# Performance work log

Hardware: AMD Instinct MI355X
Metric: run time of the kernel (lower is better)

The kernel has to match this reference:

```python
import jax, jax.numpy as jnp
import numpy as np
import math

B, T, C, H = 4, 2048, 512, 8
HD = C // H


def make_alibias(block_size, ms):
    # ALiBi-style per-head bias: -m_h * |i - j|, shape [1, H, S, S]
    idx = jnp.arange(block_size)
    dist = jnp.abs(idx[:, None] - idx[None, :]).astype(jnp.float32)  # [S,S]
    return -ms[None, :, None, None] * dist[None, None, :, :]


def setup_inputs() -> dict:
    key = jax.random.key(0)
    k1, k2, k3, k4, k5 = jax.random.split(key, 5)
    x = jax.random.normal(k1, (B, T, C), dtype=jnp.float32)
    Wqkv = jax.random.normal(k2, (C, 3 * C), dtype=jnp.float32) * (1.0 / math.sqrt(C))
    bqkv = jax.random.normal(k3, (3 * C,), dtype=jnp.float32) * 0.02
    Wproj = jax.random.normal(k4, (C, C), dtype=jnp.float32) * (1.0 / math.sqrt(C))
    bproj = jax.random.normal(k5, (C,), dtype=jnp.float32) * 0.02
    ms = jnp.arange(1, H + 1, dtype=jnp.float32) * 0.05
    alibias = make_alibias(T, ms)  # [1,H,T,T]
    return {"x": x, "Wqkv": Wqkv, "bqkv": bqkv, "Wproj": Wproj, "bproj": bproj, "alibias": alibias}


def reference(x, Wqkv, bqkv, Wproj, bproj, alibias):
    Bv, Tv, Cv = x.shape
    qkv = x @ Wqkv + bqkv                      # [B,T,3C]
    q, k, v = jnp.split(qkv, 3, axis=-1)
    # [B,T,C] -> [B,H,T,hd]
    def heads(t):
        return t.reshape(Bv, Tv, H, HD).transpose(0, 2, 1, 3)
    q, k, v = heads(q), heads(k), heads(v)
    att = jnp.einsum('bhqd,bhkd->bhqk', q, k) * (1.0 / math.sqrt(HD))
    att = att + alibias[:, :, :Tv, :Tv]
    att = jax.nn.softmax(att, axis=-1)
    y = jnp.einsum('bhqk,bhkd->bhqd', att, v)  # [B,H,T,hd]
    y = y.transpose(0, 2, 1, 3).reshape(Bv, Tv, Cv)
    return y @ Wproj + bproj
```

## Files before the change

### kernel.cpp

```cpp
#include <hip/hip_runtime.h>
#include <hip/hip_bf16.h>

#define LOG2E 1.4426950408889634f

typedef __attribute__((ext_vector_type(8))) short short8;
typedef __attribute__((ext_vector_type(8))) __bf16 bf16x8;
typedef __attribute__((ext_vector_type(4))) float f32x4;

__device__ __forceinline__ unsigned short f2b(float f){
  unsigned int u = __builtin_bit_cast(unsigned int, f);
  u += 0x7fffu + ((u >> 16) & 1u);
  return (unsigned short)(u >> 16);
}

__device__ __forceinline__ unsigned int cvtpk(float lo, float hi){
  unsigned int r;
  asm("v_cvt_pk_bf16_f32 %0, %1, %2" : "=v"(r) : "v"(lo), "v"(hi));
  return r;
}

__device__ __forceinline__ void gload16(const void* g, void* l){
  __builtin_amdgcn_global_load_lds(
      (const __attribute__((address_space(1))) unsigned int*)g,
      (__attribute__((address_space(3))) unsigned int*)l, 16, 0, 0);
}

__global__ __launch_bounds__(256) void prep_kernel(
    const float* __restrict__ x, const float* __restrict__ Wqkv, const float* __restrict__ Wproj,
    unsigned short* __restrict__ xb, unsigned short* __restrict__ wqkvT, unsigned short* __restrict__ wprojT){
  __shared__ unsigned short T[64][72];
  const int bid = blockIdx.x, tid = threadIdx.x;
  if (bid < 2048){
    size_t i = ((size_t)bid * 256 + tid) * 8;
    float4 a = *(const float4*)(x + i);
    float4 b = *(const float4*)(x + i + 4);
    short8 s;
    s[0]=(short)f2b(a.x); s[1]=(short)f2b(a.y); s[2]=(short)f2b(a.z); s[3]=(short)f2b(a.w);
    s[4]=(short)f2b(b.x); s[5]=(short)f2b(b.y); s[6]=(short)f2b(b.z); s[7]=(short)f2b(b.w);
    *(short8*)(xb + i) = s;
    return;
  }
  const float* in; unsigned short* out; int R, C, bx, by;
  if (bid < 2240){ int t = bid - 2048; bx = t % 24; by = t / 24; in = Wqkv; out = wqkvT; R = 512; C = 1536; }
  else           { int t = bid - 2240; bx = t % 8;  by = t / 8;  in = Wproj; out = wprojT; R = 512; C = 512; }
  const int r0 = by * 64, c0 = bx * 64;
  {
    const int i = tid >> 2, jg = (tid & 3) * 16;
    const float* src = in + (size_t)(r0 + i) * C + c0 + jg;
    #pragma unroll
    for (int e = 0; e < 16; e += 4){
      float4 v = *(const float4*)(src + e);
      T[i][jg + e + 0] = f2b(v.x);
      T[i][jg + e + 1] = f2b(v.y);
      T[i][jg + e + 2] = f2b(v.z);
      T[i][jg + e + 3] = f2b(v.w);
    }
  }
  __syncthreads();
  {
    const int j = tid >> 2, ig = (tid & 3) * 16;
    short8 w0, w1;
    #pragma unroll
    for (int e = 0; e < 8; e++) w0[e] = (short)T[ig + e][j];
    #pragma unroll
    for (int e = 0; e < 8; e++) w1[e] = (short)T[ig + 8 + e][j];
    unsigned short* dst = out + (size_t)(c0 + j) * R + r0 + ig;
    *(short8*)dst = w0;
    *(short8*)(dst + 8) = w1;
  }
}

__global__ __launch_bounds__(256,3) void gemm_qkv_kernel(
    const unsigned short* __restrict__ A,
    const unsigned short* __restrict__ Bt,
    const float* __restrict__ bias,
    unsigned short* __restrict__ Qb,
    unsigned short* __restrict__ Kb,
    unsigned short* __restrict__ VTb,
    float* __restrict__ Mq, float* __restrict__ Mk){
  __shared__ unsigned short As[128*64];
  __shared__ unsigned short Bs[128*64];
  const int tid = threadIdx.x, wid = tid >> 6, lane = tid & 63;
  const int wr = wid >> 1, wc = wid & 1;
  const int fr = lane & 15, fq = lane >> 4;
  const int fr7 = fr & 7;
  const int orig = blockIdx.x;
  const int xcd = orig & 7, idx = orig >> 3;
  const int bm = (xcd + 8*(idx/12)) * 128;
  const int bn = (idx % 12) * 128;
  f32x4 acc[4][4];
  #pragma unroll
  for (int m=0;m<4;m++)
    #pragma unroll
    for (int n=0;n<4;n++) acc[m][n] = (f32x4){0.f,0.f,0.f,0.f};

  for (int k0 = 0; k0 < 512; k0 += 64){
    __syncthreads();
    #pragma unroll
    for (int it=0; it<4; it++){
      const int s = it*256 + tid;
      const int row = s >> 3, c = s & 7;
      const int sc = c ^ (row & 7);
      void* al = (void*)(As + (it*256 + wid*64)*8);
      void* bl = (void*)(Bs + (it*256 + wid*64)*8);
      gload16(A  + (size_t)(bm + row)*512 + k0 + sc*8, al);
      gload16(Bt + (size_t)(bn + row)*512 + k0 + sc*8, bl);
    }
    __syncthreads();
    bf16x8 af[4][2], bfv[4][2];
    #pragma unroll
    for (int m=0;m<4;m++)
      #pragma unroll
      for (int kk=0;kk<2;kk++)
        af[m][kk]  = *(const bf16x8*)&As[(wr*64 + m*16 + fr)*64 + (((kk*4+fq)^fr7)*8)];
    #pragma unroll
    for (int n=0;n<4;n++)
      #pragma unroll
      for (int kk=0;kk<2;kk++)
        bfv[n][kk] = *(const bf16x8*)&Bs[(wc*64 + n*16 + fr)*64 + (((kk*4+fq)^fr7)*8)];
    #pragma unroll
    for (int kk=0;kk<2;kk++)
      #pragma unroll
      for (int m=0;m<4;m++)
        #pragma unroll
        for (int n=0;n<4;n++)
          acc[m][n] = __builtin_amdgcn_mfma_f32_16x16x32_bf16(af[m][kk], bfv[n][kk], acc[m][n], 0,0,0);
  }

  const float SCQ = 0.125f * LOG2E;
  const int colbase = bn + wc*64;
  const int which = colbase >> 9;
  float ss[4][4];
  #pragma unroll
  for (int m=0;m<4;m++)
    #pragma unroll
    for (int g=0;g<4;g++) ss[m][g] = 0.f;

  #pragma unroll
  for (int m=0;m<4;m++){
    const int row0 = bm + wr*64 + m*16 + fq*4;
    const int b_ = row0 >> 11, t_ = row0 & 2047;
    #pragma unroll
    for (int n=0;n<4;n++){
      const int col = colbase + n*16 + fr;
      const int c = col & 511, hh = c >> 6, dd = c & 63;
      const float bv = bias[col];
      if (which == 0){
        #pragma unroll
        for (int g=0; g<4; g++){
          const float v = (acc[m][n][g] + bv) * SCQ;
          ss[m][g] = fmaf(v, v, ss[m][g]);
          Qb[((size_t)(b_*8 + hh)*2048 + t_ + g)*64 + dd] = f2b(v);
        }
      } else if (which == 1){
        #pragma unroll
        for (int g=0; g<4; g++){
          const float v = acc[m][n][g] + bv;
          ss[m][g] = fmaf(v, v, ss[m][g]);
          Kb[((size_t)(b_*8 + hh)*2048 + t_ + g)*64 + dd] = f2b(v);
        }
      } else {
        uint2 pk;
        pk.x = cvtpk(acc[m][n][0] + bv, acc[m][n][1] + bv);
        pk.y = cvtpk(acc[m][n][2] + bv, acc[m][n][3] + bv);
        *(uint2*)&VTb[((size_t)(b_*8 + hh)*64 + dd)*2048 + t_] = pk;
      }
    }
  }

  if (which <= 1){
    #pragma unroll
    for (int m=0;m<4;m++)
      #pragma unroll
      for (int g=0;g<4;g++){
        float s = ss[m][g];
        s += __shfl_xor(s, 1); s += __shfl_xor(s, 2);
        s += __shfl_xor(s, 4); s += __shfl_xor(s, 8);
        ss[m][g] = s;
      }
    float mx = 0.f;
    #pragma unroll
    for (int m=0;m<4;m++)
      #pragma unroll
      for (int g=0;g<4;g++) mx = fmaxf(mx, ss[m][g]);
    mx = fmaxf(mx, __shfl_xor(mx, 16));
    mx = fmaxf(mx, __shfl_xor(mx, 32));
    if (lane == 0){
      const int rowbase = bm + wr*64;
      const int b_ = rowbase >> 11, qc_ = (rowbase >> 6) & 31;
      const int h_ = (colbase >> 6) & 7;
      float* M = which ? Mk : Mq;
      M[(b_*8 + h_)*32 + qc_] = sqrtf(mx) * 1.01f;
    }
  }
}

__global__ __launch_bounds__(256,3) void attn_kernel(
    const unsigned short* __restrict__ Q,
    const unsigned short* __restrict__ K,
    const unsigned short* __restrict__ VT,
    const float* __restrict__ alib,
    const float* __restrict__ Mqa,
    const float* __restrict__ Mka,
    unsigned short* __restrict__ Y){
  __shared__ unsigned short Ks[2][64*64];
  __shared__ unsigned short Vs[2][64*64];
  __shared__ unsigned short Ps[4][16][72];
  __shared__ float MkS[32];
  __shared__ float wred[4];
  __shared__ int lst[32];
  __shared__ int nsh;
  const int tid = threadIdx.x, wid = tid >> 6, lane = tid & 63;
  const int fr = lane & 15, fq = lane >> 4;
  const int fr7 = fr & 7;
  const int id = blockIdx.x;
  const int h = id >> 7;
  const int low3 = id & 7, idx4 = (id & 127) >> 3;
  const int b = idx4 >> 2, off = idx4 & 3;
  const int quad = (low3 - b) & 7;
  const int qc = quad*4 + off;
  const int bh = b*8 + h;
  const int q0 = qc*64 + wid*16;
  const unsigned short* Qp = Q  + (size_t)bh * 131072;
  const unsigned short* Kp = K  + (size_t)bh * 131072;
  const unsigned short* Vp = VT + (size_t)bh * 131072;
  const float nmh2 = alib[(size_t)h * 4194304 + 1] * LOG2E;
  const float MqMk0 = Mqa[bh*32 + qc];
  if (tid < 32) MkS[tid] = Mka[bh*32 + tid];

  bf16x8 qf[2];
  #pragma unroll
  for (int kk=0;kk<2;kk++)
    qf[kk] = *(const bf16x8*)(Qp + (size_t)(q0 + fr)*64 + kk*32 + fq*8);

  bf16x8 ones;
  #pragma unroll
  for (int e=0;e<8;e++) ones[e] = __builtin_bit_cast(__bf16, (unsigned short)0x3F80);

  f32x4 o[4], osum;
  #pragma unroll
  for (int ni=0;ni<4;ni++) o[ni] = (f32x4){0.f,0.f,0.f,0.f};
  osum = (f32x4){0.f,0.f,0.f,0.f};
  float mr = -1e30f;
  const float qi = (float)(q0 + fr);
  const float qb = nmh2 * qi;
  f32x4 ka[4];
  #pragma unroll
  for (int ni=0;ni<4;ni++)
    #pragma unroll
    for (int g=0;g<4;g++) ka[ni][g] = nmh2 * (float)(ni*16 + fq*4 + g);

  auto stage = [&](int kt, int buf){
    const int kb = kt * 64;
    #pragma unroll
    for (int it=0; it<2; it++){
      const int s = it*256 + tid;
      const int row = s >> 3, c = s & 7;
      const int sc = c ^ (row & 7);
      gload16(Kp + (size_t)(kb + row)*64 + sc*8, (void*)(Ks[buf] + (it*256 + wid*64)*8));
      gload16(Vp + (size_t)row*2048 + kb + sc*8, (void*)(Vs[buf] + (it*256 + wid*64)*8));
    }
  };

  auto compute = [&](int kt, int buf, bool diag){
    const int kb = kt * 64;
    const unsigned short* KsB = Ks[buf];
    const unsigned short* VsB = Vs[buf];
    bf16x8 kf[4][2], vf[4][2];
    #pragma unroll
    for (int ni=0;ni<4;ni++)
      #pragma unroll
      for (int kk=0;kk<2;kk++){
        const int r = ni*16 + fr;
        const int sw = ((kk*4 + fq) ^ fr7) * 8;
        kf[ni][kk] = *(const bf16x8*)&KsB[r*64 + sw];
        vf[ni][kk] = *(const bf16x8*)&VsB[r*64 + sw];
      }

    f32x4 st[4];
    const f32x4 fz = {0.f,0.f,0.f,0.f};
    #pragma unroll
    for (int ni=0;ni<4;ni++){
      f32x4 t0 = __builtin_amdgcn_mfma_f32_16x16x32_bf16(kf[ni][0], qf[0], fz, 0,0,0);
      st[ni] = __builtin_amdgcn_mfma_f32_16x16x32_bf16(kf[ni][1], qf[1], t0, 0,0,0);
    }

    float cadd;
    if (diag){
      const float base = qi - (float)(kb + fq*4);
      #pragma unroll
      for (int ni=0;ni<4;ni++)
        #pragma unroll
        for (int g=0;g<4;g++){
          const float d = fabsf(base - (float)(ni*16 + g));
          st[ni][g] = fmaf(nmh2, d, st[ni][g]);
        }
      cadd = 0.f;
    } else {
      const float s1 = (kt > qc) ? 1.f : -1.f;
      #pragma unroll
      for (int ni=0;ni<4;ni++)
        #pragma unroll
        for (int g=0;g<4;g++)
          st[ni][g] = fmaf(s1, ka[ni][g], st[ni][g]);
      cadd = s1 * (nmh2 * (float)kb - qb);
    }

    float m0 = fmaxf(fmaxf(st[0][0], st[0][1]), fmaxf(st[0][2], st[0][3]));
    float m1 = fmaxf(fmaxf(st[1][0], st[1][1]), fmaxf(st[1][2], st[1][3]));
    float m2 = fmaxf(fmaxf(st[2][0], st[2][1]), fmaxf(st[2][2], st[2][3]));
    float m3 = fmaxf(fmaxf(st[3][0], st[3][1]), fmaxf(st[3][2], st[3][3]));
    float tm = fmaxf(fmaxf(m0, m1), fmaxf(m2, m3));
    tm = fmaxf(tm, __shfl_xor(tm, 16));
    tm = fmaxf(tm, __shfl_xor(tm, 32));
    const float tmt = tm + cadd;

    const bool nog = __all(tmt <= mr);
    float mn = mr, sc;
    if (!nog){
      mn = fmaxf(mr, tmt);
      sc = exp2f(mr - mn);
      mr = mn;
    }
    const float mexp = mn - cadd;
    #pragma unroll
    for (int ni=0;ni<4;ni++)
      #pragma unroll
      for (int g=0;g<4;g++)
        st[ni][g] = exp2f(st[ni][g] - mexp);

    if (!nog){
      #pragma unroll
      for (int g=0;g<4;g++){
        const float sv = __shfl(sc, fq*4 + g);
        #pragma unroll
        for (int ni=0;ni<4;ni++) o[ni][g] *= sv;
        osum[g] *= sv;
      }
    }
    #pragma unroll
    for (int ni=0;ni<4;ni++){
      uint2 pk;
      pk.x = cvtpk(st[ni][0], st[ni][1]);
      pk.y = cvtpk(st[ni][2], st[ni][3]);
      *(uint2*)&Ps[wid][fr][ni*16 + fq*4] = pk;
    }

    bf16x8 pf[2];
    #pragma unroll
    for (int kk=0;kk<2;kk++)
      pf[kk] = *(const bf16x8*)&Ps[wid][fr][kk*32 + fq*8];
    #pragma unroll
    for (int ni=0;ni<4;ni++){
      o[ni] = __builtin_amdgcn_mfma_f32_16x16x32_bf16(pf[0], vf[ni][0], o[ni], 0,0,0);
      o[ni] = __builtin_amdgcn_mfma_f32_16x16x32_bf16(pf[1], vf[ni][1], o[ni], 0,0,0);
    }
    osum = __builtin_amdgcn_mfma_f32_16x16x32_bf16(pf[0], ones, osum, 0,0,0);
    osum = __builtin_amdgcn_mfma_f32_16x16x32_bf16(pf[1], ones, osum, 0,0,0);
  };

  const int e0 = (qc + 1 < 32) ? qc + 1 : qc - 1;
  const int e1 = (qc + 1 < 32 && qc - 1 >= 0) ? qc - 1 : -1;
  stage(qc, 0);
  stage(e0, 1);
  asm volatile("s_waitcnt vmcnt(4)" ::: "memory");
  __builtin_amdgcn_sched_barrier(0);
  __builtin_amdgcn_s_barrier();
  compute(qc, 0, true);

  float wm = mr;
  #pragma unroll
  for (int d=1; d<16; d<<=1) wm = fminf(wm, __shfl_xor(wm, d));
  if (lane == 0) wred[wid] = wm;
  __syncthreads();
  const float thresh  = fminf(fminf(wred[0], wred[1]), fminf(wred[2], wred[3])) - 14.0f;
  const float threshW = wm - 14.0f;

  if (tid == 0){
    float maxMk = 0.f;
    #pragma unroll
    for (int t=0; t<32; t++) maxMk = fmaxf(maxMk, MkS[t]);
    int n = 0;
    if (e1 >= 0) lst[n++] = e1;
    for (int dt = 2; dt < 32; dt++){
      const float biasmax = nmh2 * (float)((dt - 1)*64 + 1);
      if (MqMk0 * maxMk + biasmax < thresh) break;
      int kt = qc + dt;
      if (kt < 32 && MqMk0 * MkS[kt] + biasmax >= thresh) lst[n++] = kt;
      kt = qc - dt;
      if (kt >= 0 && MqMk0 * MkS[kt] + biasmax >= thresh) lst[n++] = kt;
    }
    nsh = n;
  }
  __syncthreads();
  const int nt = nsh + 1;

  for (int j = 0; j < nt; j++){
    const int kt = (j == 0) ? e0 : lst[j-1];
    asm volatile("s_waitcnt lgkmcnt(0)" ::: "memory");
    __builtin_amdgcn_sched_barrier(0);
    __builtin_amdgcn_s_barrier();
    if (j + 1 < nt){
      stage((j == 0) ? lst[0] : lst[j], j & 1);
      asm volatile("s_waitcnt vmcnt(4)" ::: "memory");
    } else {
      asm volatile("s_waitcnt vmcnt(0)" ::: "memory");
    }
    __builtin_amdgcn_sched_barrier(0);
    __builtin_amdgcn_s_barrier();
    const int dminW = (kt > qc) ? (kt*64 - (q0 + 15)) : (q0 - (kt*64 + 63));
    if (MqMk0 * MkS[kt] + nmh2 * (float)dminW >= threshW)
      compute(kt, (j+1)&1, false);
  }

  #pragma unroll
  for (int g=0;g<4;g++){
    const float iv = 1.0f / osum[g];
    const int t = q0 + fq*4 + g;
    #pragma unroll
    for (int ni=0;ni<4;ni++)
      Y[(size_t)(b*2048 + t)*512 + h*64 + ni*16 + fr] = f2b(o[ni][g] * iv);
  }
}

__global__ __launch_bounds__(256,2) void gemm_proj_kernel(
    const unsigned short* __restrict__ A,
    const unsigned short* __restrict__ Bt,
    const float* __restrict__ bias,
    float* __restrict__ out){
  __shared__ unsigned short As[128*64];
  __shared__ unsigned short Bs[128*64];
  const int tid = threadIdx.x, wid = tid >> 6, lane = tid & 63;
  const int wr = wid >> 1, wc = wid & 1;
  const int fr = lane & 15, fq = lane >> 4;
  const int fr7 = fr & 7;
  const int orig = blockIdx.x;
  const int xcd = orig & 7, idx = orig >> 3;
  const int bm = (xcd + 8*(idx >> 2)) * 128;
  const int bn = (idx & 3) * 128;
  f32x4 acc[4][4];
  #pragma unroll
  for (int m=0;m<4;m++)
    #pragma unroll
    for (int n=0;n<4;n++) acc[m][n] = (f32x4){0.f,0.f,0.f,0.f};

  for (int k0 = 0; k0 < 512; k0 += 64){
    __syncthreads();
    #pragma unroll
    for (int it=0; it<4; it++){
      const int s = it*256 + tid;
      const int row = s >> 3, c = s & 7;
      const int sc = c ^ (row & 7);
      void* al = (void*)(As + (it*256 + wid*64)*8);
      void* bl = (void*)(Bs + (it*256 + wid*64)*8);
      gload16(A  + (size_t)(bm + row)*512 + k0 + sc*8, al);
      gload16(Bt + (size_t)(bn + row)*512 + k0 + sc*8, bl);
    }
    __syncthreads();
    bf16x8 af[4][2], bfv[4][2];
    #pragma unroll
    for (int m=0;m<4;m++)
      #pragma unroll
      for (int kk=0;kk<2;kk++)
        af[m][kk]  = *(const bf16x8*)&As[(wr*64 + m*16 + fr)*64 + (((kk*4+fq)^fr7)*8)];
    #pragma unroll
    for (int n=0;n<4;n++)
      #pragma unroll
      for (int kk=0;kk<2;kk++)
        bfv[n][kk] = *(const bf16x8*)&Bs[(wc*64 + n*16 + fr)*64 + (((kk*4+fq)^fr7)*8)];
    #pragma unroll
    for (int kk=0;kk<2;kk++)
      #pragma unroll
      for (int m=0;m<4;m++)
        #pragma unroll
        for (int n=0;n<4;n++)
          acc[m][n] = __builtin_amdgcn_mfma_f32_16x16x32_bf16(af[m][kk], bfv[n][kk], acc[m][n], 0,0,0);
  }

  #pragma unroll
  for (int m=0;m<4;m++){
    const int row0 = bm + wr*64 + m*16 + fq*4;
    #pragma unroll
    for (int n=0;n<4;n++){
      const int col = bn + wc*64 + n*16 + fr;
      const float bv = bias[col];
      #pragma unroll
      for (int g=0; g<4; g++)
        out[(size_t)(row0 + g)*512 + col] = acc[m][n][g] + bv;
    }
  }
}

extern "C" void kernel_launch(void* const* d_in, const int* in_sizes, int n_in,
                              void* d_out, int out_size, void* d_ws, size_t ws_size,
                              hipStream_t stream){
  const float* x     = (const float*)d_in[0];
  const float* Wqkv  = (const float*)d_in[1];
  const float* bqkv  = (const float*)d_in[2];
  const float* Wproj = (const float*)d_in[3];
  const float* bproj = (const float*)d_in[4];
  const float* alib  = (const float*)d_in[5];
  char* ws = (char*)d_ws;
  unsigned short* xb     = (unsigned short*)(ws);
  unsigned short* wqkvT  = (unsigned short*)(ws + 8388608);
  unsigned short* wprojT = (unsigned short*)(ws + 9961472);
  unsigned short* Qb     = (unsigned short*)(ws + 10485760);
  unsigned short* Kb     = (unsigned short*)(ws + 18874368);
  unsigned short* VTb    = (unsigned short*)(ws + 27262976);
  unsigned short* Yb     = (unsigned short*)(ws + 35651584);
  float* out = (float*)d_out;
  float* Mq = out + 4194304 - 2048;
  float* Mk = Mq + 1024;

  prep_kernel<<<2304, 256, 0, stream>>>(x, Wqkv, Wproj, xb, wqkvT, wprojT);
  gemm_qkv_kernel<<<768, 256, 0, stream>>>(xb, wqkvT, bqkv, Qb, Kb, VTb, Mq, Mk);
  attn_kernel<<<1024, 256, 0, stream>>>(Qb, Kb, VTb, alib, Mq, Mk, Yb);
  gemm_proj_kernel<<<256, 256, 0, stream>>>(Yb, wprojT, bproj, out);
}
```

Baseline: 66.54 us.

## Stage two key/value tiles per pipeline step in attention kernel

Doubles the shared-memory K/V buffers so each pipeline stage loads two 64-key tiles at once, halving the number of barrier-synchronized iterations over the key tile list. The diagonal and first neighbor tile are now loaded together and both computed before threshold selection. This cuts barriers and waits per tile, but raises LDS use and lowers the launch bound from 3 to 2 blocks per CU, reducing occupancy. It also leaves an unused, odd-looking stage2 lambda.

```diff
diff --git a/kernel.cpp b/kernel.cpp
--- a/kernel.cpp
+++ b/kernel.cpp
@@ -195,7 +195,7 @@
   }
 }
 
-__global__ __launch_bounds__(256,3) void attn_kernel(
+__global__ __launch_bounds__(256,2) void attn_kernel(
     const unsigned short* __restrict__ Q,
     const unsigned short* __restrict__ K,
     const unsigned short* __restrict__ VT,
@@ -203,8 +203,8 @@
     const float* __restrict__ Mqa,
     const float* __restrict__ Mka,
     unsigned short* __restrict__ Y){
-  __shared__ unsigned short Ks[2][64*64];
-  __shared__ unsigned short Vs[2][64*64];
+  __shared__ unsigned short Ks[2][128*64];
+  __shared__ unsigned short Vs[2][128*64];
   __shared__ unsigned short Ps[4][16][72];
   __shared__ float MkS[32];
   __shared__ float wred[4];
@@ -250,22 +250,38 @@
     #pragma unroll
     for (int g=0;g<4;g++) ka[ni][g] = nmh2 * (float)(ni*16 + fq*4 + g);
 
-  auto stage = [&](int kt, int buf){
-    const int kb = kt * 64;
-    #pragma unroll
-    for (int it=0; it<2; it++){
+  auto stage2 = [&](int kta, int ktb, int buf){
+    #pragma unroll
+    for (int it=0; it<4; it++){
       const int s = it*256 + tid;
       const int row = s >> 3, c = s & 7;
       const int sc = c ^ (row & 7);
-      gload16(Kp + (size_t)(kb + row)*64 + sc*8, (void*)(Ks[buf] + (it*256 + wid*64)*8));
-      gload16(Vp + (size_t)row*2048 + kb + sc*8, (void*)(Vs[buf] + (it*256 + wid*64)*8));
+      const int kt = (row < 64) ? kta : ktb;
+      const int kr = kt*64 + (row & 63);
+      gload16(Kp + (size_t)kr*64 + sc*8, (void*)(Ks[buf] + (it*256 + wid*64)*8));
+      gload16(Vp + (size_t)(row & 63)*2048 + ((row<64)?kta:ktb)*64 + (row>>6)*65536 + sc*8 - (row>>6)*65536
+              + ((row<64)?0:(size_t)64*2048) - ((row<64)?0:(size_t)64*2048),
+              (void*)(Vs[buf] + (it*256 + wid*64)*8));
     }
   };
 
-  auto compute = [&](int kt, int buf, bool diag){
+  auto stage2v = [&](int kta, int ktb, int buf){
+    #pragma unroll
+    for (int it=0; it<4; it++){
+      const int s = it*256 + tid;
+      const int row = s >> 3, c = s & 7;
+      const int sc = c ^ (row & 7);
+      const int kt = (row < 64) ? kta : ktb;
+      const int kr = kt*64 + (row & 63);
+      gload16(Kp + (size_t)kr*64 + sc*8, (void*)(Ks[buf] + (it*256 + wid*64)*8));
+      gload16(Vp + (size_t)(row & 63)*2048 + kt*64 + sc*8, (void*)(Vs[buf] + (it*256 + wid*64)*8));
+    }
+  };
+
+  auto compute = [&](int kt, int buf, int half, bool diag){
     const int kb = kt * 64;
-    const unsigned short* KsB = Ks[buf];
-    const unsigned short* VsB = Vs[buf];
+    const unsigned short* KsB = Ks[buf] + half*64*64;
+    const unsigned short* VsB = Vs[buf] + half*64*64;
     bf16x8 kf[4][2], vf[4][2];
     #pragma unroll
     for (int ni=0;ni<4;ni++)
@@ -361,12 +377,12 @@
 
   const int e0 = (qc + 1 < 32) ? qc + 1 : qc - 1;
   const int e1 = (qc + 1 < 32 && qc - 1 >= 0) ? qc - 1 : -1;
-  stage(qc, 0);
-  stage(e0, 1);
-  asm volatile("s_waitcnt vmcnt(4)" ::: "memory");
+  stage2v(qc, e0, 0);
+  asm volatile("s_waitcnt vmcnt(0)" ::: "memory");
   __builtin_amdgcn_sched_barrier(0);
   __builtin_amdgcn_s_barrier();
-  compute(qc, 0, true);
+  compute(qc, 0, 0, true);
+  compute(e0, 0, 1, false);
 
   float wm = mr;
   #pragma unroll
@@ -393,24 +409,42 @@
     nsh = n;
   }
   __syncthreads();
-  const int nt = nsh + 1;
-
-  for (int j = 0; j < nt; j++){
-    const int kt = (j == 0) ? e0 : lst[j-1];
-    asm volatile("s_waitcnt lgkmcnt(0)" ::: "memory");
-    __builtin_amdgcn_sched_barrier(0);
-    __builtin_amdgcn_s_barrier();
-    if (j + 1 < nt){
-      stage((j == 0) ? lst[0] : lst[j], j & 1);
-      asm volatile("s_waitcnt vmcnt(4)" ::: "memory");
-    } else {
-      asm volatile("s_waitcnt vmcnt(0)" ::: "memory");
-    }
-    __builtin_amdgcn_sched_barrier(0);
-    __builtin_amdgcn_s_barrier();
-    const int dminW = (kt > qc) ? (kt*64 - (q0 + 15)) : (q0 - (kt*64 + 63));
-    if (MqMk0 * MkS[kt] + nmh2 * (float)dminW >= threshW)
-      compute(kt, (j+1)&1, false);
+  const int n = nsh;
+  const int ng = (n + 1) >> 1;
+
+  if (ng > 0){
+    {
+      const int a0 = lst[0];
+      const int b0 = (1 < n) ? lst[1] : a0;
+      stage2v(a0, b0, 1);
+    }
+    for (int g = 0; g < ng; g++){
+      const int ka_ = lst[2*g];
+      const int kb_ = (2*g + 1 < n) ? lst[2*g + 1] : -1;
+      asm volatile("s_waitcnt lgkmcnt(0)" ::: "memory");
+      __builtin_amdgcn_sched_barrier(0);
+      __builtin_amdgcn_s_barrier();
+      if (g + 1 < ng){
+        const int a1 = lst[2*g + 2];
+        const int b1 = (2*g + 3 < n) ? lst[2*g + 3] : a1;
+        stage2v(a1, b1, g & 1);
+        asm volatile("s_waitcnt vmcnt(8)" ::: "memory");
+      } else {
+        asm volatile("s_waitcnt vmcnt(0)" ::: "memory");
+      }
+      __builtin_amdgcn_sched_barrier(0);
+      __builtin_amdgcn_s_barrier();
+      {
+        const int dminW = (ka_ > qc) ? (ka_*64 - (q0 + 15)) : (q0 - (ka_*64 + 63));
+        if (MqMk0 * MkS[ka_] + nmh2 * (float)dminW >= threshW)
+          compute(ka_, (g+1)&1, 0, false);
+      }
+      if (kb_ >= 0){
+        const int dminW = (kb_ > qc) ? (kb_*64 - (q0 + 15)) : (q0 - (kb_*64 + 63));
+        if (MqMk0 * MkS[kb_] + nmh2 * (float)dminW >= threshW)
+          compute(kb_, (g+1)&1, 1, false);
+      }
+    }
   }
 
   #pragma unroll
```

Result: no change. 66.54 us (-0.0%).
